# Performance work log

Hardware: AMD Instinct MI355X
Metric: run time of the kernel (lower is better)

## Reference

```python
import jax, jax.numpy as jnp
import numpy as np

N_NODES = 100000


def _gcn_conv(x, W, b, src, dst, deg_inv_sqrt, n):
    # PyG GCNConv: h = x @ W; out[i] = sum_{(j->i)} norm_ji * h[j] + b
    h = x @ W                                   # [N, out_dim]
    norm = deg_inv_sqrt[src] * deg_inv_sqrt[dst]  # [E_total]
    msg = h[src] * norm[:, None]                # gather + scale
    out = jax.ops.segment_sum(msg, dst, num_segments=n)  # scatter-add
    return out + b


def setup_inputs() -> dict:
    key = jax.random.key(0)
    k1, k2, k3, k4, k5, k6 = jax.random.split(key, 6)
    num_features, hidden, embedding_size = 128, 32, 64
    n_edges = 3200000
    x = jax.random.normal(k1, (N_NODES, num_features), dtype=jnp.float32)
    edge_index = jax.random.randint(k2, (2, n_edges), 0, N_NODES, dtype=jnp.int64)
    # Glorot init like PyG GCNConv
    W1 = jax.random.normal(k3, (num_features, hidden), dtype=jnp.float32) * (1.0 / np.sqrt(num_features))
    b1 = jnp.zeros((hidden,), dtype=jnp.float32)
    W2 = jax.random.normal(k4, (hidden, embedding_size), dtype=jnp.float32) * (1.0 / np.sqrt(hidden))
    b2 = jnp.zeros((embedding_size,), dtype=jnp.float32)
    return {"x": x, "edge_index": edge_index, "W1": W1, "b1": b1, "W2": W2, "b2": b2}


def reference(x, edge_index, W1, b1, W2, b2):
    n = x.shape[0]
    # add self-loops (GCNConv default add_self_loops=True)
    loop = jnp.arange(n, dtype=edge_index.dtype)
    src = jnp.concatenate([edge_index[0], loop])
    dst = jnp.concatenate([edge_index[1], loop])
    # symmetric normalization: deg includes self-loops, edge_weight = 1
    deg = jax.ops.segment_sum(jnp.ones_like(dst, dtype=x.dtype), dst, num_segments=n)
    deg_inv_sqrt = jnp.where(deg > 0, jax.lax.rsqrt(deg), 0.0)

    h = _gcn_conv(x, W1, b1, src, dst, deg_inv_sqrt, n)
    h = jax.nn.relu(h)
    # F.dropout(p=0.2, training=False) -> identity in eval mode
    out = _gcn_conv(h, W2, b2, src, dst, deg_inv_sqrt, n)
    return out
```

## Files before the change

kernel.cpp:

```cpp
#include <hip/hip_runtime.h>
#include <hip/hip_bf16.h>


#define NF 128
#define HID 32
#define EMB 64

#define BSHIFT 10
#define BNODES 1024
#define CAP 36864
#define NBUKMAX 128
#define TILE 4096
#define EPT 16
#define CHUNKS 8

typedef float vf4 __attribute__((ext_vector_type(4)));
typedef unsigned vu4 __attribute__((ext_vector_type(4)));

static __device__ __forceinline__ unsigned bf16rne(float f) {
    unsigned u = __float_as_uint(f);
    return (u + 0x7fffu + ((u >> 16) & 1u)) >> 16;
}

static __device__ __host__ __forceinline__ int hslot(int b, int c) {
    return ((b >> 3) << 6) | (c << 3) | (b & 7);
}

#define ACC8(v) \
    a0 += __uint_as_float((v).x << 16); a1 += __uint_as_float((v).x & 0xffff0000u); \
    a2 += __uint_as_float((v).y << 16); a3 += __uint_as_float((v).y & 0xffff0000u); \
    a4 += __uint_as_float((v).z << 16); a5 += __uint_as_float((v).z & 0xffff0000u); \
    a6 += __uint_as_float((v).w << 16); a7 += __uint_as_float((v).w & 0xffff0000u);

__global__ __launch_bounds__(256) void k_part(const void* __restrict__ ei,
                                              unsigned* __restrict__ pairs,
                                              int* __restrict__ bcur,
                                              int* __restrict__ cnt_ovf,
                                              unsigned long long* __restrict__ ovf,
                                              int* __restrict__ ovfcnt,
                                              int E, int nbuk) {
    __shared__ unsigned sEnt[TILE];
    __shared__ unsigned char sB[TILE];
    __shared__ int hcntw[4][NBUKMAX];
    __shared__ int lcurw[4][NBUKMAX];
    __shared__ int lstart[NBUKMAX], gbase[NBUKMAX];
    __shared__ int sNZ;
    const int tid = threadIdx.x;
    const int w = tid >> 6;
    const int tile0 = blockIdx.x * TILE;
    if (tile0 >= E) return;
    const int tcnt = min(TILE, E - tile0);

    if (tid == 0) sNZ = 0;
    for (int b = tid; b < 4 * NBUKMAX; b += 256) {
        ((int*)hcntw)[b] = 0;
        ((int*)lcurw)[b] = 0;
    }
    __syncthreads();
    {
        int i = tile0 + tid;
        if (i < E) {
            unsigned hw = ((const unsigned*)ei)[2 * (size_t)i + 1];
            if (hw) sNZ = 1;
        }
    }
    __syncthreads();
    const bool is64 = (sNZ == 0);

    int ms[EPT], md[EPT];
#pragma unroll
    for (int k = 0; k < EPT; ++k) {
        int i = tile0 + k * 256 + tid;
        ms[k] = -1;
        if (i < tile0 + tcnt) {
            int s, d;
            if (is64) {
                const long long* p = (const long long*)ei;
                s = (int)__builtin_nontemporal_load(&p[i]);
                d = (int)__builtin_nontemporal_load(&p[(size_t)E + i]);
            } else {
                const int* p = (const int*)ei;
                s = __builtin_nontemporal_load(&p[i]);
                d = __builtin_nontemporal_load(&p[E + i]);
            }
            ms[k] = s; md[k] = d;
            atomicAdd(&hcntw[w][d >> BSHIFT], 1);
        }
    }
    __syncthreads();

    if (tid < 64) {
        int i0 = tid * 2, i1 = tid * 2 + 1;
        int c0 = 0, c1 = 0;
        if (i0 < nbuk) { c0 = hcntw[0][i0] + hcntw[1][i0] + hcntw[2][i0] + hcntw[3][i0]; }
        if (i1 < nbuk) { c1 = hcntw[0][i1] + hcntw[1][i1] + hcntw[2][i1] + hcntw[3][i1]; }
        int run = c0 + c1, inc = run;
#pragma unroll
        for (int off = 1; off < 64; off <<= 1) {
            int t2 = __shfl_up(inc, off);
            if (tid >= off) inc += t2;
        }
        int excl = inc - run;
        if (i0 < nbuk) {
            lstart[i0] = excl;
            gbase[i0] = c0 ? atomicAdd(&bcur[i0], c0) : 0;
            int off2 = excl;
#pragma unroll
            for (int ww = 0; ww < 4; ++ww) { int t3 = hcntw[ww][i0]; hcntw[ww][i0] = off2; off2 += t3; }
        }
        if (i1 < nbuk) {
            lstart[i1] = excl + c0;
            gbase[i1] = c1 ? atomicAdd(&bcur[i1], c1) : 0;
            int off2 = excl + c0;
#pragma unroll
            for (int ww = 0; ww < 4; ++ww) { int t3 = hcntw[ww][i1]; hcntw[ww][i1] = off2; off2 += t3; }
        }
    }
    __syncthreads();

#pragma unroll
    for (int k = 0; k < EPT; ++k) {
        if (ms[k] >= 0) {
            int b = md[k] >> BSHIFT;
            int slot = hcntw[w][b] + atomicAdd(&lcurw[w][b], 1);
            sEnt[slot] = ((unsigned)(md[k] & (BNODES - 1)) << 17) | (unsigned)ms[k];
            sB[slot] = (unsigned char)b;
        }
    }
    __syncthreads();

    for (int j = tid; j < tcnt; j += 256) {
        unsigned ent = sEnt[j];
        int b = sB[j];
        int g = gbase[b] + (j - lstart[b]);
        if (g < CAP) {
            pairs[(size_t)b * CAP + g] = ent;
        } else {
            int d = (b << BSHIFT) | (int)(ent >> 17);
            int s = (int)(ent & 0x1FFFFu);
            int o = atomicAdd(ovfcnt, 1);
            ovf[o] = ((unsigned long long)(unsigned)d << 32) | (unsigned)s;
            atomicAdd(&cnt_ovf[d], 1);
        }
    }
}

__global__ void k_bscan(const int* __restrict__ bcur, int* __restrict__ bbase,
                        int* __restrict__ roff, int nbuk, int E, int N) {
    __shared__ int sh[128];
    int t = threadIdx.x;
    int v = (t < nbuk) ? bcur[t] : 0;
    sh[t] = v;
    __syncthreads();
    for (int off = 1; off < 128; off <<= 1) {
        int add = (t >= off) ? sh[t - off] : 0;
        __syncthreads();
        sh[t] += add;
        __syncthreads();
    }
    if (t < nbuk) bbase[t] = sh[t] - v;
    if (t == 0) roff[N] = E;
}

__global__ __launch_bounds__(256) void k_hist(const unsigned* __restrict__ pairs,
                                              const int* __restrict__ bcur,
                                              int* __restrict__ histc, int nbuk) {
    __shared__ int hist[BNODES];
    const int idx = blockIdx.x;
    const int c = (idx >> 3) & 7;
    const int b = (idx & 7) | ((idx >> 6) << 3);
    if (b >= nbuk) return;
    const int tid = threadIdx.x;
    const int nb = min(bcur[b], CAP);
    const int csz = (nb + CHUNKS - 1) / CHUNKS;
    const int i0 = c * csz, i1 = min(nb, i0 + csz);
    const unsigned* pp = pairs + (size_t)b * CAP;
    for (int i = tid; i < BNODES; i += 256) hist[i] = 0;
    __syncthreads();
    for (int i = i0 + tid; i < i1; i += 256)
        atomicAdd(&hist[__builtin_nontemporal_load(&pp[i]) >> 17], 1);
    __syncthreads();
    int* outp = histc + ((size_t)idx << 10);
    for (int i = tid; i < BNODES; i += 256) outp[i] = hist[i];
}

__global__ __launch_bounds__(256) void k_nscan(int* __restrict__ histc,
                                               const int* __restrict__ bbase,
                                               const int* __restrict__ cnt_ovf,
                                               int* __restrict__ roff,
                                               int* __restrict__ cursor,
                                               float* __restrict__ dis, int N) {
    __shared__ int part[256];
    const int b = blockIdx.x, tid = threadIdx.x;
    const int base = bbase[b];
    int h[4][CHUNKS], stg[4], tv[4];
    int run = 0;
    const int l0 = tid * 4;
#pragma unroll
    for (int k = 0; k < 4; ++k) {
        int l = l0 + k;
        int node = (b << BSHIFT) + l;
        int st = 0;
#pragma unroll
        for (int c = 0; c < CHUNKS; ++c) {
            h[k][c] = histc[((size_t)hslot(b, c) << 10) + l];
            st += h[k][c];
        }
        stg[k] = st;
        int ov = (node < N) ? cnt_ovf[node] : 0;
        tv[k] = st + ov;
        run += tv[k];
    }
    part[tid] = run;
    __syncthreads();
    for (int off = 1; off < 256; off <<= 1) {
        int add = (tid >= off) ? part[tid - off] : 0;
        __syncthreads();
        part[tid] += add;
        __syncthreads();
    }
    int excl = part[tid] - run;
#pragma unroll
    for (int k = 0; k < 4; ++k) {
        int l = l0 + k;
        int node = (b << BSHIFT) + l;
        if (node < N) {
            roff[node] = base + excl;
            cursor[node] = base + excl + stg[k];
            dis[node] = rsqrtf((float)(tv[k] + 1));
        }
        int cb = base + excl;
#pragma unroll
        for (int c = 0; c < CHUNKS; ++c) {
            int hh = h[k][c];
            histc[((size_t)hslot(b, c) << 10) + l] = cb;
            cb += hh;
        }
        excl += tv[k];
    }
}

__global__ __launch_bounds__(256) void k_scat2(const unsigned* __restrict__ pairs,
                                               const int* __restrict__ bcur,
                                               const int* __restrict__ histc,
                                               int* __restrict__ csr, int nbuk) {
    __shared__ int cbase[BNODES];
    __shared__ int lc[BNODES];
    const int idx = blockIdx.x;
    const int c = (idx >> 3) & 7;
    const int b = (idx & 7) | ((idx >> 6) << 3);
    if (b >= nbuk) return;
    const int tid = threadIdx.x;
    const int nb = min(bcur[b], CAP);
    const int csz = (nb + CHUNKS - 1) / CHUNKS;
    const int i0 = c * csz, i1 = min(nb, i0 + csz);
    const unsigned* pp = pairs + (size_t)b * CAP;
    const int* hc = histc + ((size_t)idx << 10);
    for (int i = tid; i < BNODES; i += 256) { cbase[i] = hc[i]; lc[i] = 0; }
    __syncthreads();
    int i = i0 + tid;
    for (; i + 768 < i1; i += 1024) {
        unsigned e0 = pp[i], e1 = pp[i + 256], e2 = pp[i + 512], e3 = pp[i + 768];
        int l0 = e0 >> 17, l1 = e1 >> 17, l2 = e2 >> 17, l3 = e3 >> 17;
        int p0 = cbase[l0] + atomicAdd(&lc[l0], 1);
        int p1 = cbase[l1] + atomicAdd(&lc[l1], 1);
        int p2 = cbase[l2] + atomicAdd(&lc[l2], 1);
        int p3 = cbase[l3] + atomicAdd(&lc[l3], 1);
        csr[p0] = (int)(e0 & 0x1FFFFu);
        csr[p1] = (int)(e1 & 0x1FFFFu);
        csr[p2] = (int)(e2 & 0x1FFFFu);
        csr[p3] = (int)(e3 & 0x1FFFFu);
    }
    for (; i < i1; i += 256) {
        unsigned ent = pp[i];
        int l = ent >> 17;
        int pos = cbase[l] + atomicAdd(&lc[l], 1);
        csr[pos] = (int)(ent & 0x1FFFFu);
    }
}

__global__ __launch_bounds__(256) void k_ovf(const unsigned long long* __restrict__ ovf,
                                             const int* __restrict__ ovfcnt,
                                             int* __restrict__ cursor,
                                             int* __restrict__ csr) {
    int n = *ovfcnt;
    for (int i = blockIdx.x * 256 + threadIdx.x; i < n; i += 256 * 8) {
        unsigned long long pr = ovf[i];
        int pos = atomicAdd(&cursor[(int)(unsigned)(pr >> 32)], 1);
        csr[pos] = (int)(unsigned)pr;
    }
}

__global__ __launch_bounds__(256) void k_gemm1(const float* __restrict__ x,
                                               const float* __restrict__ W,
                                               const float* __restrict__ dis,
                                               unsigned* __restrict__ h1b, int N) {
    __shared__ float sW[NF * HID];
    __shared__ float sx[32][132];
    const int t = threadIdx.x;
    for (int i = t; i < NF * HID; i += 256) sW[i] = W[i];
    const int row0 = blockIdx.x * 32;
    {
        const float4* xv = (const float4*)(x + (size_t)row0 * NF);
        for (int i = t; i < 32 * 32; i += 256) {
            int r = i >> 5, c = i & 31;
            float4 v = make_float4(0.f, 0.f, 0.f, 0.f);
            if (row0 + r < N) v = xv[(size_t)r * 32 + c];
            *(float4*)&sx[r][c * 4] = v;
        }
    }
    __syncthreads();
    const int col4 = (t & 7) * 4;
    const int row = t >> 3;
    float a0 = 0.f, a1 = 0.f, a2 = 0.f, a3 = 0.f;
#pragma unroll 8
    for (int k = 0; k < NF; ++k) {
        float xs = sx[row][k];
        float4 w = *(const float4*)&sW[k * HID + col4];
        a0 += xs * w.x; a1 += xs * w.y; a2 += xs * w.z; a3 += xs * w.w;
    }
    int r = row0 + row;
    if (r < N) {
        float d = dis[r];
        unsigned u0 = bf16rne(a0 * d) | (bf16rne(a1 * d) << 16);
        unsigned u1 = bf16rne(a2 * d) | (bf16rne(a3 * d) << 16);
        *(uint2*)&h1b[(size_t)r * 16 + (t & 7) * 2] = make_uint2(u0, u1);
    }
}

__global__ __launch_bounds__(256) void k_agg1(const uint4* __restrict__ h1b,
                                              const int* __restrict__ roff,
                                              const int* __restrict__ csr,
                                              const float* __restrict__ dis,
                                              const float* __restrict__ b1,
                                              uint4* __restrict__ t_out, int N) {
    int tt = blockIdx.x * 256 + threadIdx.x;
    int node = tt >> 2;
    if (node >= N) return;
    int j = tt & 3;
    uint4 u = h1b[(size_t)node * 4 + j];
    float a0, a1, a2, a3, a4, a5, a6, a7;
    a0 = __uint_as_float(u.x << 16); a1 = __uint_as_float(u.x & 0xffff0000u);
    a2 = __uint_as_float(u.y << 16); a3 = __uint_as_float(u.y & 0xffff0000u);
    a4 = __uint_as_float(u.z << 16); a5 = __uint_as_float(u.z & 0xffff0000u);
    a6 = __uint_as_float(u.w << 16); a7 = __uint_as_float(u.w & 0xffff0000u);
    int e0 = roff[node], e1 = roff[node + 1];
    int e = e0;
    for (; e + 8 <= e1; e += 8) {
        int s0 = __builtin_nontemporal_load(&csr[e + 0]);
        int s1 = __builtin_nontemporal_load(&csr[e + 1]);
        int s2 = __builtin_nontemporal_load(&csr[e + 2]);
        int s3 = __builtin_nontemporal_load(&csr[e + 3]);
        int s4 = __builtin_nontemporal_load(&csr[e + 4]);
        int s5 = __builtin_nontemporal_load(&csr[e + 5]);
        int s6 = __builtin_nontemporal_load(&csr[e + 6]);
        int s7 = __builtin_nontemporal_load(&csr[e + 7]);
        uint4 v0 = h1b[(size_t)s0 * 4 + j];
        uint4 v1 = h1b[(size_t)s1 * 4 + j];
        uint4 v2 = h1b[(size_t)s2 * 4 + j];
        uint4 v3 = h1b[(size_t)s3 * 4 + j];
        uint4 v4 = h1b[(size_t)s4 * 4 + j];
        uint4 v5 = h1b[(size_t)s5 * 4 + j];
        uint4 v6 = h1b[(size_t)s6 * 4 + j];
        uint4 v7 = h1b[(size_t)s7 * 4 + j];
        ACC8(v0) ACC8(v1) ACC8(v2) ACC8(v3) ACC8(v4) ACC8(v5) ACC8(v6) ACC8(v7)
    }
    for (; e + 4 <= e1; e += 4) {
        int s0 = __builtin_nontemporal_load(&csr[e + 0]);
        int s1 = __builtin_nontemporal_load(&csr[e + 1]);
        int s2 = __builtin_nontemporal_load(&csr[e + 2]);
        int s3 = __builtin_nontemporal_load(&csr[e + 3]);
        uint4 v0 = h1b[(size_t)s0 * 4 + j];
        uint4 v1 = h1b[(size_t)s1 * 4 + j];
        uint4 v2 = h1b[(size_t)s2 * 4 + j];
        uint4 v3 = h1b[(size_t)s3 * 4 + j];
        ACC8(v0) ACC8(v1) ACC8(v2) ACC8(v3)
    }
    for (; e < e1; ++e) {
        int s = __builtin_nontemporal_load(&csr[e]);
        uint4 v = h1b[(size_t)s * 4 + j];
        ACC8(v)
    }
    float d = dis[node];
    float4 bb0 = *(const float4*)&b1[j * 8];
    float4 bb1 = *(const float4*)&b1[j * 8 + 4];
    float r0 = fmaxf(a0 * d + bb0.x, 0.f) * d, r1 = fmaxf(a1 * d + bb0.y, 0.f) * d;
    float r2 = fmaxf(a2 * d + bb0.z, 0.f) * d, r3 = fmaxf(a3 * d + bb0.w, 0.f) * d;
    float r4 = fmaxf(a4 * d + bb1.x, 0.f) * d, r5 = fmaxf(a5 * d + bb1.y, 0.f) * d;
    float r6 = fmaxf(a6 * d + bb1.z, 0.f) * d, r7 = fmaxf(a7 * d + bb1.w, 0.f) * d;
    uint4 o;
    o.x = bf16rne(r0) | (bf16rne(r1) << 16);
    o.y = bf16rne(r2) | (bf16rne(r3) << 16);
    o.z = bf16rne(r4) | (bf16rne(r5) << 16);
    o.w = bf16rne(r6) | (bf16rne(r7) << 16);
    t_out[(size_t)node * 4 + j] = o;
}

__global__ __launch_bounds__(256) void k_agg2(const uint4* __restrict__ tb,
                                              const int* __restrict__ roff,
                                              const int* __restrict__ csr,
                                              const float* __restrict__ dis,
                                              float* __restrict__ s2, int N) {
    int tt = blockIdx.x * 256 + threadIdx.x;
    int node = tt >> 2;
    if (node >= N) return;
    int j = tt & 3;
    uint4 u = tb[(size_t)node * 4 + j];
    float a0, a1, a2, a3, a4, a5, a6, a7;
    a0 = __uint_as_float(u.x << 16); a1 = __uint_as_float(u.x & 0xffff0000u);
    a2 = __uint_as_float(u.y << 16); a3 = __uint_as_float(u.y & 0xffff0000u);
    a4 = __uint_as_float(u.z << 16); a5 = __uint_as_float(u.z & 0xffff0000u);
    a6 = __uint_as_float(u.w << 16); a7 = __uint_as_float(u.w & 0xffff0000u);
    int e0 = roff[node], e1 = roff[node + 1];
    int e = e0;
    for (; e + 8 <= e1; e += 8) {
        int s0 = __builtin_nontemporal_load(&csr[e + 0]);
        int s1 = __builtin_nontemporal_load(&csr[e + 1]);
        int s2i = __builtin_nontemporal_load(&csr[e + 2]);
        int s3 = __builtin_nontemporal_load(&csr[e + 3]);
        int s4 = __builtin_nontemporal_load(&csr[e + 4]);
        int s5 = __builtin_nontemporal_load(&csr[e + 5]);
        int s6 = __builtin_nontemporal_load(&csr[e + 6]);
        int s7 = __builtin_nontemporal_load(&csr[e + 7]);
        uint4 v0 = tb[(size_t)s0 * 4 + j];
        uint4 v1 = tb[(size_t)s1 * 4 + j];
        uint4 v2 = tb[(size_t)s2i * 4 + j];
        uint4 v3 = tb[(size_t)s3 * 4 + j];
        uint4 v4 = tb[(size_t)s4 * 4 + j];
        uint4 v5 = tb[(size_t)s5 * 4 + j];
        uint4 v6 = tb[(size_t)s6 * 4 + j];
        uint4 v7 = tb[(size_t)s7 * 4 + j];
        ACC8(v0) ACC8(v1) ACC8(v2) ACC8(v3) ACC8(v4) ACC8(v5) ACC8(v6) ACC8(v7)
    }
    for (; e + 4 <= e1; e += 4) {
        int s0 = __builtin_nontemporal_load(&csr[e + 0]);
        int s1 = __builtin_nontemporal_load(&csr[e + 1]);
        int s2i = __builtin_nontemporal_load(&csr[e + 2]);
        int s3 = __builtin_nontemporal_load(&csr[e + 3]);
        uint4 v0 = tb[(size_t)s0 * 4 + j];
        uint4 v1 = tb[(size_t)s1 * 4 + j];
        uint4 v2 = tb[(size_t)s2i * 4 + j];
        uint4 v3 = tb[(size_t)s3 * 4 + j];
        ACC8(v0) ACC8(v1) ACC8(v2) ACC8(v3)
    }
    for (; e < e1; ++e) {
        int s = __builtin_nontemporal_load(&csr[e]);
        uint4 v = tb[(size_t)s * 4 + j];
        ACC8(v)
    }
    float d = dis[node];
    vf4 o0, o1;
    o0.x = a0 * d; o0.y = a1 * d; o0.z = a2 * d; o0.w = a3 * d;
    o1.x = a4 * d; o1.y = a5 * d; o1.z = a6 * d; o1.w = a7 * d;
    vf4* op = (vf4*)&s2[(size_t)node * HID + j * 8];
    __builtin_nontemporal_store(o0, op);
    __builtin_nontemporal_store(o1, op + 1);
}

__global__ __launch_bounds__(256) void k_gemm2(const float* __restrict__ a,
                                               const float* __restrict__ W,
                                               const float* __restrict__ b2,
                                               float* __restrict__ out, int N) {
    __shared__ float sW[HID * EMB];
    __shared__ float sx[32][36];
    const int t = threadIdx.x;
    for (int i = t; i < HID * EMB; i += 256) sW[i] = W[i];
    const int row0 = blockIdx.x * 32;
    {
        const float4* av = (const float4*)(a + (size_t)row0 * HID);
        int r = t >> 3, c = t & 7;
        float4 v = make_float4(0.f, 0.f, 0.f, 0.f);
        if (row0 + r < N) v = av[(size_t)r * 8 + c];
        *(float4*)&sx[r][c * 4] = v;
    }
    __syncthreads();
    const int col4 = (t & 15) * 4;
    const int r0 = t >> 4;
    float a00 = 0.f, a01 = 0.f, a02 = 0.f, a03 = 0.f;
    float a10 = 0.f, a11 = 0.f, a12 = 0.f, a13 = 0.f;
#pragma unroll
    for (int k = 0; k < HID; ++k) {
        float4 w = *(const float4*)&sW[k * EMB + col4];
        float xa = sx[r0][k];
        float xb = sx[r0 + 16][k];
        a00 += xa * w.x; a01 += xa * w.y; a02 += xa * w.z; a03 += xa * w.w;
        a10 += xb * w.x; a11 += xb * w.y; a12 += xb * w.z; a13 += xb * w.w;
    }
    float4 bb = *(const float4*)&b2[col4];
    int ra = row0 + r0, rb = row0 + r0 + 16;
    if (ra < N) {
        vf4 o; o.x = a00 + bb.x; o.y = a01 + bb.y; o.z = a02 + bb.z; o.w = a03 + bb.w;
        __builtin_nontemporal_store(o, (vf4*)&out[(size_t)ra * EMB + col4]);
    }
    if (rb < N) {
        vf4 o; o.x = a10 + bb.x; o.y = a11 + bb.y; o.z = a12 + bb.z; o.w = a13 + bb.w;
        __builtin_nontemporal_store(o, (vf4*)&out[(size_t)rb * EMB + col4]);
    }
}

extern "C" void kernel_launch(void* const* d_in, const int* in_sizes, int n_in,
                              void* d_out, int out_size, void* d_ws, size_t ws_size,
                              hipStream_t stream) {
    const float* x  = (const float*)d_in[0];
    const void*  ei = d_in[1];
    const float* W1 = (const float*)d_in[2];
    const float* b1 = (const float*)d_in[3];
    const float* W2 = (const float*)d_in[4];
    const float* b2 = (const float*)d_in[5];
    float* out = (float*)d_out;

    const int N = in_sizes[0] / NF;
    const int E = in_sizes[1] / 2;
    const int nbuk = (N + BNODES - 1) >> BSHIFT;

    char* ws = (char*)d_ws;
    size_t off = 0;
    auto take = [&](size_t bytes) -> void* {
        void* p = ws + off;
        off += (bytes + 255) & ~(size_t)255;
        return p;
    };
    int* cnt_ovf = (int*)take((size_t)N * 4);
    int* bcur    = (int*)take((size_t)NBUKMAX * 4);
    int* ovfcnt  = (int*)take(4);
    size_t zbytes = off;
    int*                bbase  = (int*)take((size_t)NBUKMAX * 4);
    int*                roff   = (int*)take((size_t)(N + 1) * 4);
    int*                cursor = (int*)take((size_t)N * 4);
    float*              dis    = (float*)take((size_t)N * 4);
    int*                histc  = (int*)take((size_t)NBUKMAX * CHUNKS * BNODES * 4);
    unsigned*           pairs  = (unsigned*)take((size_t)nbuk * CAP * 4);
    unsigned long long* ovf    = (unsigned long long*)take((size_t)E * 8);
    int*                csr    = (int*)take((size_t)E * 4);
    unsigned*           h1b    = (unsigned*)take((size_t)N * HID * 2);
    unsigned*           tb     = (unsigned*)take((size_t)N * HID * 2);
    float*              s2     = (float*)take((size_t)N * HID * 4);

    (void)hipMemsetAsync(cnt_ovf, 0, zbytes, stream);

    const int gridBC = ((nbuk + 7) / 8) * 64;
    const int gridAgg = (int)(((size_t)N * 4 + 255) / 256);

    k_part<<<(E + TILE - 1) / TILE, 256, 0, stream>>>(ei, pairs, bcur, cnt_ovf,
                                                      ovf, ovfcnt, E, nbuk);
    k_bscan<<<1, 128, 0, stream>>>(bcur, bbase, roff, nbuk, E, N);
    k_hist<<<gridBC, 256, 0, stream>>>(pairs, bcur, histc, nbuk);
    k_nscan<<<nbuk, 256, 0, stream>>>(histc, bbase, cnt_ovf, roff, cursor, dis, N);
    k_scat2<<<gridBC, 256, 0, stream>>>(pairs, bcur, histc, csr, nbuk);
    k_ovf<<<8, 256, 0, stream>>>(ovf, ovfcnt, cursor, csr);

    k_gemm1<<<(N + 31) / 32, 256, 0, stream>>>(x, W1, dis, h1b, N);
    k_agg1<<<gridAgg, 256, 0, stream>>>((const uint4*)h1b, roff, csr, dis, b1,
                                        (uint4*)tb, N);
    k_agg2<<<gridAgg, 256, 0, stream>>>((const uint4*)tb, roff, csr, dis, s2, N);
    k_gemm2<<<(N + 31) / 32, 256, 0, stream>>>(s2, W2, b2, out, N);
}
```

Measured before the change: 232.5 us.

## Split hidden features into two half-width planes and aggregate each plane separately

The bf16 hidden features are stored as two separate 16-channel planes instead of one 32-channel array. Each aggregation layer now runs as two passes, one per plane, with two threads per node instead of four. Each plane is half the size, so the random gathers should hit L2/MALL more often. The cost is reading the CSR index arrays twice and launching extra kernels. It also clamps the chunk start index in the histogram and scatter kernels so it cannot pass the bucket size.

```diff
diff --git a/kernel.cpp b/kernel.cpp
--- a/kernel.cpp
+++ b/kernel.cpp
@@ -173,7 +173,7 @@
     const int tid = threadIdx.x;
     const int nb = min(bcur[b], CAP);
     const int csz = (nb + CHUNKS - 1) / CHUNKS;
-    const int i0 = c * csz, i1 = min(nb, i0 + csz);
+    const int i0 = min(nb, c * csz), i1 = min(nb, i0 + csz);
     const unsigned* pp = pairs + (size_t)b * CAP;
     for (int i = tid; i < BNODES; i += 256) hist[i] = 0;
     __syncthreads();
@@ -253,7 +253,7 @@
     const int tid = threadIdx.x;
     const int nb = min(bcur[b], CAP);
     const int csz = (nb + CHUNKS - 1) / CHUNKS;
-    const int i0 = c * csz, i1 = min(nb, i0 + csz);
+    const int i0 = min(nb, c * csz), i1 = min(nb, i0 + csz);
     const unsigned* pp = pairs + (size_t)b * CAP;
     const int* hc = histc + ((size_t)idx << 10);
     for (int i = tid; i < BNODES; i += 256) { cbase[i] = hc[i]; lc[i] = 0; }
@@ -294,7 +294,8 @@
 __global__ __launch_bounds__(256) void k_gemm1(const float* __restrict__ x,
                                                const float* __restrict__ W,
                                                const float* __restrict__ dis,
-                                               unsigned* __restrict__ h1b, int N) {
+                                               unsigned* __restrict__ h1b0,
+                                               unsigned* __restrict__ h1b1, int N) {
     __shared__ float sW[NF * HID];
     __shared__ float sx[32][132];
     const int t = threadIdx.x;
@@ -324,21 +325,22 @@
         float d = dis[r];
         unsigned u0 = bf16rne(a0 * d) | (bf16rne(a1 * d) << 16);
         unsigned u1 = bf16rne(a2 * d) | (bf16rne(a3 * d) << 16);
-        *(uint2*)&h1b[(size_t)r * 16 + (t & 7) * 2] = make_uint2(u0, u1);
-    }
-}
-
-__global__ __launch_bounds__(256) void k_agg1(const uint4* __restrict__ h1b,
-                                              const int* __restrict__ roff,
-                                              const int* __restrict__ csr,
-                                              const float* __restrict__ dis,
-                                              const float* __restrict__ b1,
-                                              uint4* __restrict__ t_out, int N) {
+        unsigned* dst = ((t & 7) < 4) ? h1b0 : h1b1;
+        *(uint2*)&dst[(size_t)r * 8 + ((t & 7) & 3) * 2] = make_uint2(u0, u1);
+    }
+}
+
+__global__ __launch_bounds__(256) void k_agg1s(const uint4* __restrict__ hs,
+                                               const int* __restrict__ roff,
+                                               const int* __restrict__ csr,
+                                               const float* __restrict__ dis,
+                                               const float* __restrict__ b1p,
+                                               uint4* __restrict__ tbp, int N) {
     int tt = blockIdx.x * 256 + threadIdx.x;
-    int node = tt >> 2;
+    int node = tt >> 1;
     if (node >= N) return;
-    int j = tt & 3;
-    uint4 u = h1b[(size_t)node * 4 + j];
+    int j = tt & 1;
+    uint4 u = hs[(size_t)node * 2 + j];
     float a0, a1, a2, a3, a4, a5, a6, a7;
     a0 = __uint_as_float(u.x << 16); a1 = __uint_as_float(u.x & 0xffff0000u);
     a2 = __uint_as_float(u.y << 16); a3 = __uint_as_float(u.y & 0xffff0000u);
@@ -355,14 +357,14 @@
         int s5 = __builtin_nontemporal_load(&csr[e + 5]);
         int s6 = __builtin_nontemporal_load(&csr[e + 6]);
         int s7 = __builtin_nontemporal_load(&csr[e + 7]);
-        uint4 v0 = h1b[(size_t)s0 * 4 + j];
-        uint4 v1 = h1b[(size_t)s1 * 4 + j];
-        uint4 v2 = h1b[(size_t)s2 * 4 + j];
-        uint4 v3 = h1b[(size_t)s3 * 4 + j];
-        uint4 v4 = h1b[(size_t)s4 * 4 + j];
-        uint4 v5 = h1b[(size_t)s5 * 4 + j];
-        uint4 v6 = h1b[(size_t)s6 * 4 + j];
-        uint4 v7 = h1b[(size_t)s7 * 4 + j];
+        uint4 v0 = hs[(size_t)s0 * 2 + j];
+        uint4 v1 = hs[(size_t)s1 * 2 + j];
+        uint4 v2 = hs[(size_t)s2 * 2 + j];
+        uint4 v3 = hs[(size_t)s3 * 2 + j];
+        uint4 v4 = hs[(size_t)s4 * 2 + j];
+        uint4 v5 = hs[(size_t)s5 * 2 + j];
+        uint4 v6 = hs[(size_t)s6 * 2 + j];
+        uint4 v7 = hs[(size_t)s7 * 2 + j];
         ACC8(v0) ACC8(v1) ACC8(v2) ACC8(v3) ACC8(v4) ACC8(v5) ACC8(v6) ACC8(v7)
     }
     for (; e + 4 <= e1; e += 4) {
@@ -370,20 +372,20 @@
         int s1 = __builtin_nontemporal_load(&csr[e + 1]);
         int s2 = __builtin_nontemporal_load(&csr[e + 2]);
         int s3 = __builtin_nontemporal_load(&csr[e + 3]);
-        uint4 v0 = h1b[(size_t)s0 * 4 + j];
-        uint4 v1 = h1b[(size_t)s1 * 4 + j];
-        uint4 v2 = h1b[(size_t)s2 * 4 + j];
-        uint4 v3 = h1b[(size_t)s3 * 4 + j];
+        uint4 v0 = hs[(size_t)s0 * 2 + j];
+        uint4 v1 = hs[(size_t)s1 * 2 + j];
+        uint4 v2 = hs[(size_t)s2 * 2 + j];
+        uint4 v3 = hs[(size_t)s3 * 2 + j];
         ACC8(v0) ACC8(v1) ACC8(v2) ACC8(v3)
     }
     for (; e < e1; ++e) {
         int s = __builtin_nontemporal_load(&csr[e]);
-        uint4 v = h1b[(size_t)s * 4 + j];
+        uint4 v = hs[(size_t)s * 2 + j];
         ACC8(v)
     }
     float d = dis[node];
-    float4 bb0 = *(const float4*)&b1[j * 8];
-    float4 bb1 = *(const float4*)&b1[j * 8 + 4];
+    float4 bb0 = *(const float4*)&b1p[j * 8];
+    float4 bb1 = *(const float4*)&b1p[j * 8 + 4];
     float r0 = fmaxf(a0 * d + bb0.x, 0.f) * d, r1 = fmaxf(a1 * d + bb0.y, 0.f) * d;
     float r2 = fmaxf(a2 * d + bb0.z, 0.f) * d, r3 = fmaxf(a3 * d + bb0.w, 0.f) * d;
     float r4 = fmaxf(a4 * d + bb1.x, 0.f) * d, r5 = fmaxf(a5 * d + bb1.y, 0.f) * d;
@@ -393,19 +395,20 @@
     o.y = bf16rne(r2) | (bf16rne(r3) << 16);
     o.z = bf16rne(r4) | (bf16rne(r5) << 16);
     o.w = bf16rne(r6) | (bf16rne(r7) << 16);
-    t_out[(size_t)node * 4 + j] = o;
-}
-
-__global__ __launch_bounds__(256) void k_agg2(const uint4* __restrict__ tb,
-                                              const int* __restrict__ roff,
-                                              const int* __restrict__ csr,
-                                              const float* __restrict__ dis,
-                                              float* __restrict__ s2, int N) {
+    tbp[(size_t)node * 2 + j] = o;
+}
+
+__global__ __launch_bounds__(256) void k_agg2s(const uint4* __restrict__ tbp,
+                                               const int* __restrict__ roff,
+                                               const int* __restrict__ csr,
+                                               const float* __restrict__ dis,
+                                               float* __restrict__ s2,
+                                               int chbase, int N) {
     int tt = blockIdx.x * 256 + threadIdx.x;
-    int node = tt >> 2;
+    int node = tt >> 1;
     if (node >= N) return;
-    int j = tt & 3;
-    uint4 u = tb[(size_t)node * 4 + j];
+    int j = tt & 1;
+    uint4 u = tbp[(size_t)node * 2 + j];
     float a0, a1, a2, a3, a4, a5, a6, a7;
     a0 = __uint_as_float(u.x << 16); a1 = __uint_as_float(u.x & 0xffff0000u);
     a2 = __uint_as_float(u.y << 16); a3 = __uint_as_float(u.y & 0xffff0000u);
@@ -422,14 +425,14 @@
         int s5 = __builtin_nontemporal_load(&csr[e + 5]);
         int s6 = __builtin_nontemporal_load(&csr[e + 6]);
         int s7 = __builtin_nontemporal_load(&csr[e + 7]);
-        uint4 v0 = tb[(size_t)s0 * 4 + j];
-        uint4 v1 = tb[(size_t)s1 * 4 + j];
-        uint4 v2 = tb[(size_t)s2i * 4 + j];
-        uint4 v3 = tb[(size_t)s3 * 4 + j];
-        uint4 v4 = tb[(size_t)s4 * 4 + j];
-        uint4 v5 = tb[(size_t)s5 * 4 + j];
-        uint4 v6 = tb[(size_t)s6 * 4 + j];
-        uint4 v7 = tb[(size_t)s7 * 4 + j];
+        uint4 v0 = tbp[(size_t)s0 * 2 + j];
+        uint4 v1 = tbp[(size_t)s1 * 2 + j];
+        uint4 v2 = tbp[(size_t)s2i * 2 + j];
+        uint4 v3 = tbp[(size_t)s3 * 2 + j];
+        uint4 v4 = tbp[(size_t)s4 * 2 + j];
+        uint4 v5 = tbp[(size_t)s5 * 2 + j];
+        uint4 v6 = tbp[(size_t)s6 * 2 + j];
+        uint4 v7 = tbp[(size_t)s7 * 2 + j];
         ACC8(v0) ACC8(v1) ACC8(v2) ACC8(v3) ACC8(v4) ACC8(v5) ACC8(v6) ACC8(v7)
     }
     for (; e + 4 <= e1; e += 4) {
@@ -437,22 +440,22 @@
         int s1 = __builtin_nontemporal_load(&csr[e + 1]);
         int s2i = __builtin_nontemporal_load(&csr[e + 2]);
         int s3 = __builtin_nontemporal_load(&csr[e + 3]);
-        uint4 v0 = tb[(size_t)s0 * 4 + j];
-        uint4 v1 = tb[(size_t)s1 * 4 + j];
-        uint4 v2 = tb[(size_t)s2i * 4 + j];
-        uint4 v3 = tb[(size_t)s3 * 4 + j];
+        uint4 v0 = tbp[(size_t)s0 * 2 + j];
+        uint4 v1 = tbp[(size_t)s1 * 2 + j];
+        uint4 v2 = tbp[(size_t)s2i * 2 + j];
+        uint4 v3 = tbp[(size_t)s3 * 2 + j];
         ACC8(v0) ACC8(v1) ACC8(v2) ACC8(v3)
     }
     for (; e < e1; ++e) {
         int s = __builtin_nontemporal_load(&csr[e]);
-        uint4 v = tb[(size_t)s * 4 + j];
+        uint4 v = tbp[(size_t)s * 2 + j];
         ACC8(v)
     }
     float d = dis[node];
     vf4 o0, o1;
     o0.x = a0 * d; o0.y = a1 * d; o0.z = a2 * d; o0.w = a3 * d;
     o1.x = a4 * d; o1.y = a5 * d; o1.z = a6 * d; o1.w = a7 * d;
-    vf4* op = (vf4*)&s2[(size_t)node * HID + j * 8];
+    vf4* op = (vf4*)&s2[(size_t)node * HID + chbase + j * 8];
     __builtin_nontemporal_store(o0, op);
     __builtin_nontemporal_store(o1, op + 1);
 }
@@ -532,14 +535,16 @@
     unsigned*           pairs  = (unsigned*)take((size_t)nbuk * CAP * 4);
     unsigned long long* ovf    = (unsigned long long*)take((size_t)E * 8);
     int*                csr    = (int*)take((size_t)E * 4);
-    unsigned*           h1b    = (unsigned*)take((size_t)N * HID * 2);
-    unsigned*           tb     = (unsigned*)take((size_t)N * HID * 2);
+    unsigned*           h1b0   = (unsigned*)take((size_t)N * 16 * 2);
+    unsigned*           h1b1   = (unsigned*)take((size_t)N * 16 * 2);
+    unsigned*           tb0    = (unsigned*)take((size_t)N * 16 * 2);
+    unsigned*           tb1    = (unsigned*)take((size_t)N * 16 * 2);
     float*              s2     = (float*)take((size_t)N * HID * 4);
 
     (void)hipMemsetAsync(cnt_ovf, 0, zbytes, stream);
 
     const int gridBC = ((nbuk + 7) / 8) * 64;
-    const int gridAgg = (int)(((size_t)N * 4 + 255) / 256);
+    const int gridAgg = (int)(((size_t)N * 2 + 255) / 256);
 
     k_part<<<(E + TILE - 1) / TILE, 256, 0, stream>>>(ei, pairs, bcur, cnt_ovf,
                                                       ovf, ovfcnt, E, nbuk);
@@ -549,9 +554,14 @@
     k_scat2<<<gridBC, 256, 0, stream>>>(pairs, bcur, histc, csr, nbuk);
     k_ovf<<<8, 256, 0, stream>>>(ovf, ovfcnt, cursor, csr);
 
-    k_gemm1<<<(N + 31) / 32, 256, 0, stream>>>(x, W1, dis, h1b, N);
-    k_agg1<<<gridAgg, 256, 0, stream>>>((const uint4*)h1b, roff, csr, dis, b1,
-                                        (uint4*)tb, N);
-    k_agg2<<<gridAgg, 256, 0, stream>>>((const uint4*)tb, roff, csr, dis, s2, N);
+    k_gemm1<<<(N + 31) / 32, 256, 0, stream>>>(x, W1, dis, h1b0, h1b1, N);
+    k_agg1s<<<gridAgg, 256, 0, stream>>>((const uint4*)h1b0, roff, csr, dis,
+                                         b1, (uint4*)tb0, N);
+    k_agg1s<<<gridAgg, 256, 0, stream>>>((const uint4*)h1b1, roff, csr, dis,
+                                         b1 + 16, (uint4*)tb1, N);
+    k_agg2s<<<gridAgg, 256, 0, stream>>>((const uint4*)tb0, roff, csr, dis,
+                                         s2, 0, N);
+    k_agg2s<<<gridAgg, 256, 0, stream>>>((const uint4*)tb1, roff, csr, dis,
+                                         s2, 16, N);
     k_gemm2<<<(N + 31) / 32, 256, 0, stream>>>(s2, W2, b2, out, N);
 }
```

Result: slower. 291.4 us (+25.3%).

## Shard bucket counters into 8 sub-regions and fold overflow pass into scatter

Applied to the files above, without the earlier changes.

Each bucket's global atomic counter is split into 8 counters selected by block index, and each gets its own sub-region of the pairs buffer. This spreads atomic contention across more addresses, and the hist and scatter chunks now map directly onto those sub-regions. The separate overflow kernel is merged into k_scat2, which removes one launch. A risk is that per-sub-region capacity (CAPS) is reached more easily, sending more edges down the slower overflow path. The merged overflow loop also runs concurrently with the scatter, which is safe only because overflow positions are reserved through cursor.

```diff
diff --git a/kernel.cpp b/kernel.cpp
--- a/kernel.cpp
+++ b/kernel.cpp
@@ -8,7 +8,8 @@
 
 #define BSHIFT 10
 #define BNODES 1024
-#define CAP 36864
+#define CAPS 4608
+#define CAP (8 * CAPS)
 #define NBUKMAX 128
 #define TILE 4096
 #define EPT 16
@@ -34,7 +35,7 @@
 
 __global__ __launch_bounds__(256) void k_part(const void* __restrict__ ei,
                                               unsigned* __restrict__ pairs,
-                                              int* __restrict__ bcur,
+                                              int* __restrict__ bcur8,
                                               int* __restrict__ cnt_ovf,
                                               unsigned long long* __restrict__ ovf,
                                               int* __restrict__ ovfcnt,
@@ -47,6 +48,7 @@
     __shared__ int sNZ;
     const int tid = threadIdx.x;
     const int w = tid >> 6;
+    const int grp = blockIdx.x & 7;
     const int tile0 = blockIdx.x * TILE;
     if (tile0 >= E) return;
     const int tcnt = min(TILE, E - tile0);
@@ -103,14 +105,14 @@
         int excl = inc - run;
         if (i0 < nbuk) {
             lstart[i0] = excl;
-            gbase[i0] = c0 ? atomicAdd(&bcur[i0], c0) : 0;
+            gbase[i0] = c0 ? atomicAdd(&bcur8[i0 * 8 + grp], c0) : 0;
             int off2 = excl;
 #pragma unroll
             for (int ww = 0; ww < 4; ++ww) { int t3 = hcntw[ww][i0]; hcntw[ww][i0] = off2; off2 += t3; }
         }
         if (i1 < nbuk) {
             lstart[i1] = excl + c0;
-            gbase[i1] = c1 ? atomicAdd(&bcur[i1], c1) : 0;
+            gbase[i1] = c1 ? atomicAdd(&bcur8[i1 * 8 + grp], c1) : 0;
             int off2 = excl + c0;
 #pragma unroll
             for (int ww = 0; ww < 4; ++ww) { int t3 = hcntw[ww][i1]; hcntw[ww][i1] = off2; off2 += t3; }
@@ -133,8 +135,8 @@
         unsigned ent = sEnt[j];
         int b = sB[j];
         int g = gbase[b] + (j - lstart[b]);
-        if (g < CAP) {
-            pairs[(size_t)b * CAP + g] = ent;
+        if (g < CAPS) {
+            pairs[(size_t)b * CAP + grp * CAPS + g] = ent;
         } else {
             int d = (b << BSHIFT) | (int)(ent >> 17);
             int s = (int)(ent & 0x1FFFFu);
@@ -145,11 +147,15 @@
     }
 }
 
-__global__ void k_bscan(const int* __restrict__ bcur, int* __restrict__ bbase,
+__global__ void k_bscan(const int* __restrict__ bcur8, int* __restrict__ bbase,
                         int* __restrict__ roff, int nbuk, int E, int N) {
     __shared__ int sh[128];
     int t = threadIdx.x;
-    int v = (t < nbuk) ? bcur[t] : 0;
+    int v = 0;
+    if (t < nbuk) {
+#pragma unroll
+        for (int k = 0; k < 8; ++k) v += bcur8[t * 8 + k];
+    }
     sh[t] = v;
     __syncthreads();
     for (int off = 1; off < 128; off <<= 1) {
@@ -163,7 +169,7 @@
 }
 
 __global__ __launch_bounds__(256) void k_hist(const unsigned* __restrict__ pairs,
-                                              const int* __restrict__ bcur,
+                                              const int* __restrict__ bcur8,
                                               int* __restrict__ histc, int nbuk) {
     __shared__ int hist[BNODES];
     const int idx = blockIdx.x;
@@ -171,9 +177,8 @@
     const int b = (idx & 7) | ((idx >> 6) << 3);
     if (b >= nbuk) return;
     const int tid = threadIdx.x;
-    const int nb = min(bcur[b], CAP);
-    const int csz = (nb + CHUNKS - 1) / CHUNKS;
-    const int i0 = c * csz, i1 = min(nb, i0 + csz);
+    const int nbc = min(bcur8[b * 8 + c], CAPS);
+    const int i0 = c * CAPS, i1 = i0 + nbc;
     const unsigned* pp = pairs + (size_t)b * CAP;
     for (int i = tid; i < BNODES; i += 256) hist[i] = 0;
     __syncthreads();
@@ -241,50 +246,47 @@
 }
 
 __global__ __launch_bounds__(256) void k_scat2(const unsigned* __restrict__ pairs,
-                                               const int* __restrict__ bcur,
+                                               const int* __restrict__ bcur8,
                                                const int* __restrict__ histc,
-                                               int* __restrict__ csr, int nbuk) {
+                                               int* __restrict__ csr,
+                                               const unsigned long long* __restrict__ ovf,
+                                               const int* __restrict__ ovfcnt,
+                                               int* __restrict__ cursor, int nbuk) {
     __shared__ int cbase[BNODES];
     __shared__ int lc[BNODES];
     const int idx = blockIdx.x;
     const int c = (idx >> 3) & 7;
     const int b = (idx & 7) | ((idx >> 6) << 3);
-    if (b >= nbuk) return;
     const int tid = threadIdx.x;
-    const int nb = min(bcur[b], CAP);
-    const int csz = (nb + CHUNKS - 1) / CHUNKS;
-    const int i0 = c * csz, i1 = min(nb, i0 + csz);
-    const unsigned* pp = pairs + (size_t)b * CAP;
-    const int* hc = histc + ((size_t)idx << 10);
-    for (int i = tid; i < BNODES; i += 256) { cbase[i] = hc[i]; lc[i] = 0; }
-    __syncthreads();
-    int i = i0 + tid;
-    for (; i + 768 < i1; i += 1024) {
-        unsigned e0 = pp[i], e1 = pp[i + 256], e2 = pp[i + 512], e3 = pp[i + 768];
-        int l0 = e0 >> 17, l1 = e1 >> 17, l2 = e2 >> 17, l3 = e3 >> 17;
-        int p0 = cbase[l0] + atomicAdd(&lc[l0], 1);
-        int p1 = cbase[l1] + atomicAdd(&lc[l1], 1);
-        int p2 = cbase[l2] + atomicAdd(&lc[l2], 1);
-        int p3 = cbase[l3] + atomicAdd(&lc[l3], 1);
-        csr[p0] = (int)(e0 & 0x1FFFFu);
-        csr[p1] = (int)(e1 & 0x1FFFFu);
-        csr[p2] = (int)(e2 & 0x1FFFFu);
-        csr[p3] = (int)(e3 & 0x1FFFFu);
-    }
-    for (; i < i1; i += 256) {
-        unsigned ent = pp[i];
-        int l = ent >> 17;
-        int pos = cbase[l] + atomicAdd(&lc[l], 1);
-        csr[pos] = (int)(ent & 0x1FFFFu);
-    }
-}
-
-__global__ __launch_bounds__(256) void k_ovf(const unsigned long long* __restrict__ ovf,
-                                             const int* __restrict__ ovfcnt,
-                                             int* __restrict__ cursor,
-                                             int* __restrict__ csr) {
+    if (b < nbuk) {
+        const int nbc = min(bcur8[b * 8 + c], CAPS);
+        const int i0 = c * CAPS, i1 = i0 + nbc;
+        const unsigned* pp = pairs + (size_t)b * CAP;
+        const int* hc = histc + ((size_t)idx << 10);
+        for (int i = tid; i < BNODES; i += 256) { cbase[i] = hc[i]; lc[i] = 0; }
+        __syncthreads();
+        int i = i0 + tid;
+        for (; i + 768 < i1; i += 1024) {
+            unsigned e0 = pp[i], e1 = pp[i + 256], e2 = pp[i + 512], e3 = pp[i + 768];
+            int l0 = e0 >> 17, l1 = e1 >> 17, l2 = e2 >> 17, l3 = e3 >> 17;
+            int p0 = cbase[l0] + atomicAdd(&lc[l0], 1);
+            int p1 = cbase[l1] + atomicAdd(&lc[l1], 1);
+            int p2 = cbase[l2] + atomicAdd(&lc[l2], 1);
+            int p3 = cbase[l3] + atomicAdd(&lc[l3], 1);
+            csr[p0] = (int)(e0 & 0x1FFFFu);
+            csr[p1] = (int)(e1 & 0x1FFFFu);
+            csr[p2] = (int)(e2 & 0x1FFFFu);
+            csr[p3] = (int)(e3 & 0x1FFFFu);
+        }
+        for (; i < i1; i += 256) {
+            unsigned ent = pp[i];
+            int l = ent >> 17;
+            int pos = cbase[l] + atomicAdd(&lc[l], 1);
+            csr[pos] = (int)(ent & 0x1FFFFu);
+        }
+    }
     int n = *ovfcnt;
-    for (int i = blockIdx.x * 256 + threadIdx.x; i < n; i += 256 * 8) {
+    for (int i = idx * 256 + tid; i < n; i += gridDim.x * 256) {
         unsigned long long pr = ovf[i];
         int pos = atomicAdd(&cursor[(int)(unsigned)(pr >> 32)], 1);
         csr[pos] = (int)(unsigned)pr;
@@ -521,7 +523,7 @@
         return p;
     };
     int* cnt_ovf = (int*)take((size_t)N * 4);
-    int* bcur    = (int*)take((size_t)NBUKMAX * 4);
+    int* bcur8   = (int*)take((size_t)NBUKMAX * 8 * 4);
     int* ovfcnt  = (int*)take(4);
     size_t zbytes = off;
     int*                bbase  = (int*)take((size_t)NBUKMAX * 4);
@@ -541,13 +543,13 @@
     const int gridBC = ((nbuk + 7) / 8) * 64;
     const int gridAgg = (int)(((size_t)N * 4 + 255) / 256);
 
-    k_part<<<(E + TILE - 1) / TILE, 256, 0, stream>>>(ei, pairs, bcur, cnt_ovf,
+    k_part<<<(E + TILE - 1) / TILE, 256, 0, stream>>>(ei, pairs, bcur8, cnt_ovf,
                                                       ovf, ovfcnt, E, nbuk);
-    k_bscan<<<1, 128, 0, stream>>>(bcur, bbase, roff, nbuk, E, N);
-    k_hist<<<gridBC, 256, 0, stream>>>(pairs, bcur, histc, nbuk);
+    k_bscan<<<1, 128, 0, stream>>>(bcur8, bbase, roff, nbuk, E, N);
+    k_hist<<<gridBC, 256, 0, stream>>>(pairs, bcur8, histc, nbuk);
     k_nscan<<<nbuk, 256, 0, stream>>>(histc, bbase, cnt_ovf, roff, cursor, dis, N);
-    k_scat2<<<gridBC, 256, 0, stream>>>(pairs, bcur, histc, csr, nbuk);
-    k_ovf<<<8, 256, 0, stream>>>(ovf, ovfcnt, cursor, csr);
+    k_scat2<<<gridBC, 256, 0, stream>>>(pairs, bcur8, histc, csr, ovf, ovfcnt,
+                                        cursor, nbuk);
 
     k_gemm1<<<(N + 31) / 32, 256, 0, stream>>>(x, W1, dis, h1b, N);
     k_agg1<<<gridAgg, 256, 0, stream>>>((const uint4*)h1b, roff, csr, dis, b1,
```

New measurement: 231.6 us. Within noise of the previous version (-0.4%).
